# Optimization experiments

Hardware: AMD Instinct MI355X
Metric: run time of the kernel (lower is better)

Reference implementation:

```python
import jax, jax.numpy as jnp
import numpy as np

D_K = 64

def setup_inputs() -> dict:
    key = jax.random.key(0)
    ks = jax.random.split(key, 9)
    B, S, D = 8, 2048, 512
    d_k, d_v = 64, 64
    return {
        "q_in": jax.random.normal(ks[0], (B, S, D), jnp.float32),
        "k_in": jax.random.normal(ks[1], (B, S, D), jnp.float32),
        "v_in": jax.random.normal(ks[2], (B, S, D), jnp.float32),
        "Wq": jax.random.normal(ks[3], (D, d_k), jnp.float32) * 0.05,
        "bq": jax.random.normal(ks[4], (d_k,), jnp.float32) * 0.05,
        "Wk": jax.random.normal(ks[5], (D, d_k), jnp.float32) * 0.05,
        "bk": jax.random.normal(ks[6], (d_k,), jnp.float32) * 0.05,
        "Wv": jax.random.normal(ks[7], (D, d_v), jnp.float32) * 0.05,
        "bv": jax.random.normal(ks[8], (d_v,), jnp.float32) * 0.05,
    }

def reference(q_in, k_in, v_in, Wq, bq, Wk, bk, Wv, bv):
    # Dense projections: x @ W + b
    q = jnp.einsum('bsd,dk->bsk', q_in, Wq) + bq  # [B,S,d_k]
    k = jnp.einsum('bsd,dk->bsk', k_in, Wk) + bk  # [B,S,d_k]
    v = jnp.einsum('bsd,dv->bsv', v_in, Wv) + bv  # [B,S,d_v]
    scale = 1.0 / np.sqrt(D_K).astype(np.float32)
    scores = jnp.einsum('bqk,bsk->bqs', q, k) * scale  # [B,S,S]
    attn = jax.nn.softmax(scores, axis=-1)
    return jnp.einsum('bqs,bsv->bqv', attn, v)  # [B,S,d_v]
```

## Files before the change

### kernel.cpp

```cpp
#include <hip/hip_runtime.h>
#include <hip/hip_bf16.h>
#include <cstdint>

typedef __attribute__((ext_vector_type(8))) short short8;
typedef __attribute__((ext_vector_type(16))) float f32x16;

#if __has_builtin(__builtin_amdgcn_exp2f)
#define EXP2F(x) __builtin_amdgcn_exp2f(x)
#else
#define EXP2F(x) exp2f(x)
#endif

#define MFMA32(A, B, C) __builtin_amdgcn_mfma_f32_32x32x16_bf16((A), (B), (C), 0, 0, 0)

__device__ __forceinline__ unsigned short f2bf(float f) {
  unsigned int u = __builtin_bit_cast(unsigned int, f);
  u += 0x7FFFu + ((u >> 16) & 1u);
  return (unsigned short)(u >> 16);
}

__global__ __launch_bounds__(256) void prep_wt(
    const float* __restrict__ Wq, const float* __restrict__ Wk,
    const float* __restrict__ Wv, unsigned short* __restrict__ Wt)
{
  int idx = blockIdx.x * 256 + threadIdx.x;
  int which = idx >> 15;
  int rem = idx & 32767;
  int n = rem >> 9;
  int k = rem & 511;
  const float* W = (which == 0) ? Wq : (which == 1) ? Wk : Wv;
  Wt[idx] = f2bf(W[k * 64 + n]);
}

__global__ __launch_bounds__(256, 3) void proj_kernel(
    const float* __restrict__ qin, const float* __restrict__ kin,
    const float* __restrict__ vin, const unsigned short* __restrict__ Wt,
    const float* __restrict__ bq, const float* __restrict__ bk,
    const float* __restrict__ bv,
    unsigned short* __restrict__ Qo, unsigned short* __restrict__ Ko,
    unsigned short* __restrict__ Vto)
{
  __shared__ unsigned short Xs[2][64 * 136];

  const int which = blockIdx.y;
  const float* X    = (which == 0) ? qin : (which == 1) ? kin : vin;
  const float* bias = (which == 0) ? bq  : (which == 1) ? bk  : bv;

  const int tid = threadIdx.x;
  const int lane = tid & 63, wv = tid >> 6;
  const int h = lane >> 5, l31 = lane & 31;
  const int grp = wv & 1, nh = wv >> 1;
  const int m0 = blockIdx.x * 64;

  const unsigned short* wcol =
      Wt + (size_t)which * 64 * 512 + (size_t)(nh * 32 + l31) * 512 + h * 8;

  const int srow = tid >> 5;
  const int skoff = tid & 31;
  const float* xg = X + (size_t)(m0 + srow) * 512 + skoff * 4;

  float4 ld[8];
  #pragma unroll
  for (int j = 0; j < 8; ++j)
    ld[j] = *(const float4*)(xg + (size_t)(8 * j) * 512);
  #pragma unroll
  for (int j = 0; j < 8; ++j) {
    unsigned int w0 = (unsigned int)f2bf(ld[j].x) | ((unsigned int)f2bf(ld[j].y) << 16);
    unsigned int w1 = (unsigned int)f2bf(ld[j].z) | ((unsigned int)f2bf(ld[j].w) << 16);
    uint2 pw; pw.x = w0; pw.y = w1;
    *(uint2*)(&Xs[0][(srow + 8 * j) * 136 + skoff * 4]) = pw;
  }
  __syncthreads();

  f32x16 acc = {};
  for (int c = 0; c < 4; ++c) {
    if (c < 3) {
      #pragma unroll
      for (int j = 0; j < 8; ++j)
        ld[j] = *(const float4*)(xg + (size_t)(8 * j) * 512 + (c + 1) * 128);
    }
    const unsigned short* arow = &Xs[c & 1][(grp * 32 + l31) * 136 + h * 8];
    const unsigned short* wk = wcol + c * 128;
    #pragma unroll
    for (int ks = 0; ks < 8; ++ks) {
      short8 af = *(const short8*)(arow + ks * 16);
      short8 bf = *(const short8*)(wk + ks * 16);
      acc = MFMA32(af, bf, acc);
    }
    if (c < 3) {
      #pragma unroll
      for (int j = 0; j < 8; ++j) {
        unsigned int w0 = (unsigned int)f2bf(ld[j].x) | ((unsigned int)f2bf(ld[j].y) << 16);
        unsigned int w1 = (unsigned int)f2bf(ld[j].z) | ((unsigned int)f2bf(ld[j].w) << 16);
        uint2 pw; pw.x = w0; pw.y = w1;
        *(uint2*)(&Xs[(c + 1) & 1][(srow + 8 * j) * 136 + skoff * 4]) = pw;
      }
      __syncthreads();
    }
  }

  const float bv0 = bias[nh * 32 + l31];

  if (which < 2) {
    const float scale = which ? 1.0f : 0.18033688f;
    unsigned short* Y = which ? Ko : Qo;
    #pragma unroll
    for (int r = 0; r < 16; ++r) {
      int row = (r & 3) + 8 * (r >> 2) + 4 * h;
      Y[(size_t)(m0 + grp * 32 + row) * 64 + nh * 32 + l31] =
          f2bf((acc[r] + bv0) * scale);
    }
  } else {
    __syncthreads();
    unsigned short* TB = &Xs[0][0];
    #pragma unroll
    for (int r = 0; r < 16; ++r) {
      int row = (r & 3) + 8 * (r >> 2) + 4 * h;
      TB[(nh * 32 + l31) * 68 + grp * 32 + row] = f2bf(acc[r] + bv0);
    }
    __syncthreads();
    int bidx = blockIdx.x >> 5;
    int s0 = (blockIdx.x & 31) * 64;
    for (int i = tid; i < 64 * 16; i += 256) {
      int n = i >> 4, cs = i & 15;
      ushort4 v4 = *(const ushort4*)(TB + n * 68 + cs * 4);
      *(ushort4*)(Vto + ((size_t)bidx * 64 + n) * 2048 + s0 + cs * 4) = v4;
    }
  }
}

__global__ __launch_bounds__(512, 2) void attn_kernel(
    const unsigned short* __restrict__ Q, const unsigned short* __restrict__ K,
    const unsigned short* __restrict__ Vt, float* __restrict__ out)
{
  __shared__ float ObS[4][16][64];
  __shared__ float MpS[4][64];
  __shared__ float LpS[4][64];

  const int tid = threadIdx.x;
  const int lane = tid & 63, w = tid >> 6;
  const int h = lane >> 5, l31 = lane & 31;
  const int b = blockIdx.y;
  const int q0 = blockIdx.x * 64;

  short8 qf[2][4];
  #pragma unroll
  for (int qt = 0; qt < 2; ++qt) {
    const unsigned short* qp = Q + ((size_t)(b * 2048 + q0 + qt * 32 + l31)) * 64 + h * 8;
    #pragma unroll
    for (int c = 0; c < 4; ++c) qf[qt][c] = *(const short8*)(qp + c * 16);
  }

  f32x16 o00 = {}, o01 = {}, o10 = {}, o11 = {};
  float m0 = -1e30f, m1 = -1e30f, ls0 = 0.f, ls1 = 0.f;

  const unsigned short* Kp  = K  + ((size_t)(b * 2048 + w * 256 + l31)) * 64 + h * 8;
  const unsigned short* Vp0 = Vt + ((size_t)(b * 64 + l31)) * 2048 + w * 256 + h * 8;
  const unsigned short* Vp1 = Vp0 + (size_t)32 * 2048;

  short8 kf[4], vf0[2], vf1[2];
  #pragma unroll
  for (int c = 0; c < 4; ++c) kf[c] = *(const short8*)(Kp + c * 16);
  vf0[0] = *(const short8*)(Vp0); vf0[1] = *(const short8*)(Vp0 + 16);
  vf1[0] = *(const short8*)(Vp1); vf1[1] = *(const short8*)(Vp1 + 16);

  auto process = [&](f32x16 sT, float &m, float &ls, f32x16 &oA, f32x16 &oB) {
    float tm[8];
    #pragma unroll
    for (int i = 0; i < 8; ++i) tm[i] = fmaxf(sT[2 * i], sT[2 * i + 1]);
    #pragma unroll
    for (int i = 0; i < 4; ++i) tm[i] = fmaxf(tm[i], tm[i + 4]);
    float mx = fmaxf(fmaxf(tm[0], tm[1]), fmaxf(tm[2], tm[3]));
    mx = fmaxf(mx, __shfl_xor(mx, 32, 64));
    if (__any(mx > m + 8.0f)) {
      float mnew = fmaxf(m, mx);
      float alpha = EXP2F(m - mnew);
      m = mnew;
      ls *= alpha; oA *= alpha; oB *= alpha;
    }
    float p[16];
    #pragma unroll
    for (int r = 0; r < 16; ++r) p[r] = EXP2F(sT[r] - m);
    float ts[8];
    #pragma unroll
    for (int i = 0; i < 8; ++i) ts[i] = p[2 * i] + p[2 * i + 1];
    #pragma unroll
    for (int i = 0; i < 4; ++i) ts[i] += ts[i + 4];
    float rs = (ts[0] + ts[1]) + (ts[2] + ts[3]);
    rs += __shfl_xor(rs, 32, 64);
    ls += rs;
    unsigned int pk[8];
    #pragma unroll
    for (int i = 0; i < 8; ++i)
      pk[i] = (unsigned int)f2bf(p[2 * i]) | ((unsigned int)f2bf(p[2 * i + 1]) << 16);
    unsigned int ex[8];
    #pragma unroll
    for (int i = 0; i < 8; ++i) ex[i] = (unsigned int)__shfl_xor((int)pk[i], 32, 64);
    uint4 cc0, cc1;
    if (h == 0) { cc0 = make_uint4(pk[0], pk[1], ex[0], ex[1]); cc1 = make_uint4(pk[4], pk[5], ex[4], ex[5]); }
    else        { cc0 = make_uint4(ex[2], ex[3], pk[2], pk[3]); cc1 = make_uint4(ex[6], ex[7], pk[6], pk[7]); }
    short8 P0 = __builtin_bit_cast(short8, cc0);
    short8 P1 = __builtin_bit_cast(short8, cc1);
    __builtin_amdgcn_s_setprio(1);
    oA = MFMA32(vf0[0], P0, oA); oA = MFMA32(vf0[1], P1, oA);
    oB = MFMA32(vf1[0], P0, oB); oB = MFMA32(vf1[1], P1, oB);
    __builtin_amdgcn_s_setprio(0);
  };

  for (int st = 0; st < 8; ++st) {
    f32x16 s0 = {}, s1 = {};
    __builtin_amdgcn_s_setprio(1);
    #pragma unroll
    for (int c = 0; c < 4; ++c) s0 = MFMA32(kf[c], qf[0][c], s0);
    #pragma unroll
    for (int c = 0; c < 4; ++c) s1 = MFMA32(kf[c], qf[1][c], s1);
    __builtin_amdgcn_s_setprio(0);
    if (st < 7) {
      #pragma unroll
      for (int c = 0; c < 4; ++c)
        kf[c] = *(const short8*)(Kp + (size_t)(st + 1) * 2048 + c * 16);
    }
    process(s0, m0, ls0, o00, o10);
    process(s1, m1, ls1, o01, o11);
    if (st < 7) {
      vf0[0] = *(const short8*)(Vp0 + (st + 1) * 32);
      vf0[1] = *(const short8*)(Vp0 + (st + 1) * 32 + 16);
      vf1[0] = *(const short8*)(Vp1 + (st + 1) * 32);
      vf1[1] = *(const short8*)(Vp1 + (st + 1) * 32 + 16);
    }
  }

  for (int half = 4; half > 0; half >>= 1) {
    const bool writer = (w >= half) && (w < 2 * half);
    const bool merger = (w < half);
    __syncthreads();
    if (writer && h == 0) {
      MpS[w - half][l31] = m0;      LpS[w - half][l31] = ls0;
      MpS[w - half][32 + l31] = m1; LpS[w - half][32 + l31] = ls1;
    }
    __syncthreads();
    float fb0 = 0.f, fb1 = 0.f;
    if (merger) {
      float pm0 = MpS[w][l31],      pl0 = LpS[w][l31];
      float pm1 = MpS[w][32 + l31], pl1 = LpS[w][32 + l31];
      float nm0 = fmaxf(m0, pm0), nm1 = fmaxf(m1, pm1);
      float fa0 = EXP2F(m0 - nm0); fb0 = EXP2F(pm0 - nm0);
      float fa1 = EXP2F(m1 - nm1); fb1 = EXP2F(pm1 - nm1);
      m0 = nm0; m1 = nm1;
      ls0 = ls0 * fa0 + pl0 * fb0; ls1 = ls1 * fa1 + pl1 * fb1;
      o00 *= fa0; o10 *= fa0; o01 *= fa1; o11 *= fa1;
    }
    __syncthreads();
    if (writer) {
      #pragma unroll
      for (int r = 0; r < 16; ++r) ObS[w - half][r][lane] = o00[r]; }
    __syncthreads();
    if (merger) {
      #pragma unroll
      for (int r = 0; r < 16; ++r) o00[r] += ObS[w][r][lane] * fb0; }
    __syncthreads();
    if (writer) {
      #pragma unroll
      for (int r = 0; r < 16; ++r) ObS[w - half][r][lane] = o01[r]; }
    __syncthreads();
    if (merger) {
      #pragma unroll
      for (int r = 0; r < 16; ++r) o01[r] += ObS[w][r][lane] * fb1; }
    __syncthreads();
    if (writer) {
      #pragma unroll
      for (int r = 0; r < 16; ++r) ObS[w - half][r][lane] = o10[r]; }
    __syncthreads();
    if (merger) {
      #pragma unroll
      for (int r = 0; r < 16; ++r) o10[r] += ObS[w][r][lane] * fb0; }
    __syncthreads();
    if (writer) {
      #pragma unroll
      for (int r = 0; r < 16; ++r) ObS[w - half][r][lane] = o11[r]; }
    __syncthreads();
    if (merger) {
      #pragma unroll
      for (int r = 0; r < 16; ++r) o11[r] += ObS[w][r][lane] * fb1; }
  }

  if (w == 0) {
    float i0 = 1.0f / ls0, i1 = 1.0f / ls1;
    o00 *= i0; o10 *= i0; o01 *= i1; o11 *= i1;
    #pragma unroll
    for (int qt = 0; qt < 2; ++qt) {
      int q = qt * 32 + l31;
      float* ob = out + ((size_t)(b * 2048 + q0 + q)) * 64 + 4 * h;
      const f32x16 a = qt ? o01 : o00;
      const f32x16 c = qt ? o11 : o10;
      #pragma unroll
      for (int g = 0; g < 4; ++g) {
        *(float4*)(ob + 8 * g)      = make_float4(a[4*g], a[4*g+1], a[4*g+2], a[4*g+3]);
        *(float4*)(ob + 32 + 8 * g) = make_float4(c[4*g], c[4*g+1], c[4*g+2], c[4*g+3]);
      }
    }
  }
}

extern "C" void kernel_launch(void* const* d_in, const int* in_sizes, int n_in,
                              void* d_out, int out_size, void* d_ws, size_t ws_size,
                              hipStream_t stream) {
  const float* qin = (const float*)d_in[0];
  const float* kin = (const float*)d_in[1];
  const float* vin = (const float*)d_in[2];
  const float* Wq  = (const float*)d_in[3];
  const float* bq  = (const float*)d_in[4];
  const float* Wk  = (const float*)d_in[5];
  const float* bk  = (const float*)d_in[6];
  const float* Wv  = (const float*)d_in[7];
  const float* bv  = (const float*)d_in[8];

  unsigned short* Qo  = (unsigned short*)d_ws;
  unsigned short* Ko  = Qo + (size_t)16384 * 64;
  unsigned short* Vto = Ko + (size_t)16384 * 64;
  unsigned short* Wt  = Vto + (size_t)8 * 64 * 2048;
  float* out = (float*)d_out;

  hipLaunchKernelGGL(prep_wt, dim3(384), dim3(256), 0, stream, Wq, Wk, Wv, Wt);
  hipLaunchKernelGGL(proj_kernel, dim3(256, 3), dim3(256), 0, stream,
                     qin, kin, vin, Wt, bq, bk, bv, Qo, Ko, Vto);
  hipLaunchKernelGGL(attn_kernel, dim3(32, 8), dim3(512), 0, stream, Qo, Ko, Vto, out);
}
```

Measured before the change: 161.4 us.

## Split attention over two key halves with a separate reduction kernel

Adds a z grid dimension so each attention block handles half of the key sequence, doubling the number of blocks to fill more of the GPU. Each block writes unnormalized partial outputs plus running max and sum to workspace, and a new reduce kernel combines the two halves with a log-sum-exp merge. This costs extra global traffic for the partials and one more kernel launch.

Measured after the change: 171.4 us. 6.2% more time.

```diff
diff --git a/kernel.cpp b/kernel.cpp
--- a/kernel.cpp
+++ b/kernel.cpp
@@ -131,7 +131,9 @@
 
 __global__ __launch_bounds__(512, 2) void attn_kernel(
     const unsigned short* __restrict__ Q, const unsigned short* __restrict__ K,
-    const unsigned short* __restrict__ Vt, float* __restrict__ out)
+    const unsigned short* __restrict__ Vt,
+    float* __restrict__ PartO, float* __restrict__ PartM,
+    float* __restrict__ PartL)
 {
   __shared__ float ObS[4][16][64];
   __shared__ float MpS[4][64];
@@ -142,6 +144,8 @@
   const int h = lane >> 5, l31 = lane & 31;
   const int b = blockIdx.y;
   const int q0 = blockIdx.x * 64;
+  const int kz = blockIdx.z;
+  const int kbase = kz * 1024 + w * 128;
 
   short8 qf[2][4];
   #pragma unroll
@@ -154,8 +158,8 @@
   f32x16 o00 = {}, o01 = {}, o10 = {}, o11 = {};
   float m0 = -1e30f, m1 = -1e30f, ls0 = 0.f, ls1 = 0.f;
 
-  const unsigned short* Kp  = K  + ((size_t)(b * 2048 + w * 256 + l31)) * 64 + h * 8;
-  const unsigned short* Vp0 = Vt + ((size_t)(b * 64 + l31)) * 2048 + w * 256 + h * 8;
+  const unsigned short* Kp  = K  + ((size_t)(b * 2048 + kbase + l31)) * 64 + h * 8;
+  const unsigned short* Vp0 = Vt + ((size_t)(b * 64 + l31)) * 2048 + kbase + h * 8;
   const unsigned short* Vp1 = Vp0 + (size_t)32 * 2048;
 
   short8 kf[4], vf0[2], vf1[2];
@@ -207,7 +211,7 @@
     __builtin_amdgcn_s_setprio(0);
   };
 
-  for (int st = 0; st < 8; ++st) {
+  for (int st = 0; st < 4; ++st) {
     f32x16 s0 = {}, s1 = {};
     __builtin_amdgcn_s_setprio(1);
     #pragma unroll
@@ -215,14 +219,14 @@
     #pragma unroll
     for (int c = 0; c < 4; ++c) s1 = MFMA32(kf[c], qf[1][c], s1);
     __builtin_amdgcn_s_setprio(0);
-    if (st < 7) {
+    if (st < 3) {
       #pragma unroll
       for (int c = 0; c < 4; ++c)
         kf[c] = *(const short8*)(Kp + (size_t)(st + 1) * 2048 + c * 16);
     }
     process(s0, m0, ls0, o00, o10);
     process(s1, m1, ls1, o01, o11);
-    if (st < 7) {
+    if (st < 3) {
       vf0[0] = *(const short8*)(Vp0 + (st + 1) * 32);
       vf0[1] = *(const short8*)(Vp0 + (st + 1) * 32 + 16);
       vf1[0] = *(const short8*)(Vp1 + (st + 1) * 32);
@@ -285,12 +289,12 @@
   }
 
   if (w == 0) {
-    float i0 = 1.0f / ls0, i1 = 1.0f / ls1;
-    o00 *= i0; o10 *= i0; o01 *= i1; o11 *= i1;
+    float* po = PartO + (size_t)kz * 16384 * 64;
     #pragma unroll
     for (int qt = 0; qt < 2; ++qt) {
       int q = qt * 32 + l31;
-      float* ob = out + ((size_t)(b * 2048 + q0 + q)) * 64 + 4 * h;
+      int gq = b * 2048 + q0 + q;
+      float* ob = po + (size_t)gq * 64 + 4 * h;
       const f32x16 a = qt ? o01 : o00;
       const f32x16 c = qt ? o11 : o10;
       #pragma unroll
@@ -298,8 +302,34 @@
         *(float4*)(ob + 8 * g)      = make_float4(a[4*g], a[4*g+1], a[4*g+2], a[4*g+3]);
         *(float4*)(ob + 32 + 8 * g) = make_float4(c[4*g], c[4*g+1], c[4*g+2], c[4*g+3]);
       }
-    }
-  }
+      if (h == 0) {
+        PartM[kz * 16384 + gq] = qt ? m1 : m0;
+        PartL[kz * 16384 + gq] = qt ? ls1 : ls0;
+      }
+    }
+  }
+}
+
+__global__ __launch_bounds__(256) void attn_reduce(
+    const float* __restrict__ PartO, const float* __restrict__ PartM,
+    const float* __restrict__ PartL, float* __restrict__ out)
+{
+  int idx = blockIdx.x * 256 + threadIdx.x;
+  int gq = idx >> 4;
+  int d4 = idx & 15;
+  float m0 = PartM[gq], m1 = PartM[16384 + gq];
+  float l0 = PartL[gq], l1 = PartL[16384 + gq];
+  float M = fmaxf(m0, m1);
+  float e0 = EXP2F(m0 - M), e1 = EXP2F(m1 - M);
+  float inv = 1.0f / (l0 * e0 + l1 * e1);
+  float4 O0 = *(const float4*)(PartO + (size_t)gq * 64 + d4 * 4);
+  float4 O1 = *(const float4*)(PartO + (size_t)16384 * 64 + (size_t)gq * 64 + d4 * 4);
+  float4 o;
+  o.x = (O0.x * e0 + O1.x * e1) * inv;
+  o.y = (O0.y * e0 + O1.y * e1) * inv;
+  o.z = (O0.z * e0 + O1.z * e1) * inv;
+  o.w = (O0.w * e0 + O1.w * e1) * inv;
+  *(float4*)(out + (size_t)gq * 64 + d4 * 4) = o;
 }
 
 extern "C" void kernel_launch(void* const* d_in, const int* in_sizes, int n_in,
@@ -319,10 +349,16 @@
   unsigned short* Ko  = Qo + (size_t)16384 * 64;
   unsigned short* Vto = Ko + (size_t)16384 * 64;
   unsigned short* Wt  = Vto + (size_t)8 * 64 * 2048;
+  float* PartO = (float*)(Wt + (size_t)3 * 64 * 512);
+  float* PartM = PartO + (size_t)2 * 16384 * 64;
+  float* PartL = PartM + (size_t)2 * 16384;
   float* out = (float*)d_out;
 
   hipLaunchKernelGGL(prep_wt, dim3(384), dim3(256), 0, stream, Wq, Wk, Wv, Wt);
   hipLaunchKernelGGL(proj_kernel, dim3(256, 3), dim3(256), 0, stream,
                      qin, kin, vin, Wt, bq, bk, bv, Qo, Ko, Vto);
-  hipLaunchKernelGGL(attn_kernel, dim3(32, 8), dim3(512), 0, stream, Qo, Ko, Vto, out);
-}
+  hipLaunchKernelGGL(attn_kernel, dim3(32, 8, 2), dim3(512), 0, stream,
+                     Qo, Ko, Vto, PartO, PartM, PartL);
+  hipLaunchKernelGGL(attn_reduce, dim3(1024), dim3(256), 0, stream,
+                     PartO, PartM, PartL, out);
+}
```
